# Kernel tuning notes

Measured on AMD Instinct MI355X. Metric: run time of the kernel, lower is better.

The kernel has to match this reference:

```python
import jax, jax.numpy as jnp
import numpy as np

N, D = 8192, 64


def setup_inputs() -> dict:
    key = jax.random.key(0)
    k1, k2, k3 = jax.random.split(key, 3)
    X = jax.random.normal(k1, (N, D), dtype=jnp.float32)
    target = jax.random.normal(k2, (N,), dtype=jnp.float32)
    params = jax.random.uniform(k3, (D,), dtype=jnp.float32)  # positive ARD weights
    return {"X": X, "target": target, "params": params}


def reference(X, target, params):
    # ARD-RBF kernel: k(x, y) = exp(-sum(params * (x - y)^2))
    # = exp(-||xs - ys||^2) with xs = x * sqrt(params)
    Xs = X * jnp.sqrt(params)  # [N, D]
    sq = jnp.sum(Xs * Xs, axis=-1)  # [N]
    d2 = jnp.maximum(sq[:, None] + sq[None, :] - 2.0 * (Xs @ Xs.T), 0.0)  # [N, N]
    K = jnp.exp(-d2)
    # torch version initializes K = eye(N) and never overwrites the diagonal
    n = X.shape[0]
    K = K.at[jnp.arange(n), jnp.arange(n)].set(1.0)
    K_target = jnp.outer(target, target)  # [N, N]
    kta = jnp.sum(K * K_target) / (n * jnp.sqrt(jnp.sum(K * K)))
    return -kta
```

## Files before the change

### kernel.cpp

```cpp
#include <hip/hip_runtime.h>
#include <hip/hip_bf16.h>

#define NROWS 8192
#define DIM 64
#define NT 64
#define NTRI (NT * (NT + 1) / 2)

typedef __attribute__((ext_vector_type(8))) short short8;
typedef __attribute__((ext_vector_type(4))) float f32x4;

static constexpr float LOG2E = 1.4426950408889634f;

#if defined(__has_builtin) && __has_builtin(__builtin_amdgcn_exp2f)
#define EXP2F(x) __builtin_amdgcn_exp2f(x)
#else
#define EXP2F(x) exp2f(x)
#endif

__global__ __launch_bounds__(256) void prep_kernel(const float* __restrict__ X,
                                                   const float* __restrict__ params,
                                                   const float* __restrict__ t,
                                                   float2* __restrict__ Lt,
                                                   short* __restrict__ Xp) {
    int tid  = threadIdx.x;
    int wave = tid >> 6, lane = tid & 63;
    int r8 = lane >> 3, c = lane & 7;
    int row = blockIdx.x * 32 + wave * 8 + r8;

    const float* xr = X + row * DIM + c * 8;
    float4 x0 = *(const float4*)xr;
    float4 x1 = *(const float4*)(xr + 4);
    float4 p0 = *(const float4*)(params + c * 8);
    float4 p1 = *(const float4*)(params + c * 8 + 4);

    float v[8];
    v[0] = x0.x * sqrtf(p0.x); v[1] = x0.y * sqrtf(p0.y);
    v[2] = x0.z * sqrtf(p0.z); v[3] = x0.w * sqrtf(p0.w);
    v[4] = x1.x * sqrtf(p1.x); v[5] = x1.y * sqrtf(p1.y);
    v[6] = x1.z * sqrtf(p1.z); v[7] = x1.w * sqrtf(p1.w);

    short8 h;
    float s = 0.f;
    #pragma unroll
    for (int i = 0; i < 8; ++i) {
        __hip_bfloat16 b = __float2bfloat16(v[i]);
        union { __hip_bfloat16 bb; short ss; } u; u.bb = b;
        h[i] = u.ss;
        float bf = __bfloat162float(b);
        s += bf * bf;
    }
    int panel = row >> 4, pr = row & 15;
    ((short8*)Xp)[panel * 128 + c * 16 + pr] = h;

    #pragma unroll
    for (int m = 1; m < 8; m <<= 1) s += __shfl_xor(s, m, 64);
    if (c == 0) Lt[row] = make_float2(LOG2E * s, t[row]);
}

__global__ __launch_bounds__(256, 4) void kta_main(const short* __restrict__ Xp,
                                                   const float2* __restrict__ Lt,
                                                   float2* __restrict__ partial) {
    int k = blockIdx.x;
    int it = (int)((129.0f - sqrtf(16641.0f - 8.0f * (float)k)) * 0.5f);
    if (it > NT - 1) it = NT - 1;
    while ((it * (129 - it)) / 2 > k) --it;
    while (((it + 1) * (128 - it)) / 2 <= k) ++it;
    int jt = it + (k - (it * (129 - it)) / 2);

    int tid  = threadIdx.x;
    int wave = tid >> 6, lane = tid & 63;
    int quad = lane >> 4, l16 = lane & 15;
    int rbase = it * 128 + (wave >> 1) * 64;
    int cbase = jt * 128 + (wave & 1) * 64;
    int pA0 = rbase >> 4, pB0 = cbase >> 4;

    const short8* Xpv = (const short8*)Xp;

    float negLC[4], tC[4];
    #pragma unroll
    for (int ct = 0; ct < 4; ++ct) {
        float2 lc = Lt[cbase + ct * 16 + l16];
        negLC[ct] = -lc.x;
        tC[ct]    = lc.y;
    }

    f32x4 c[4][4];
    #pragma unroll
    for (int rt = 0; rt < 4; ++rt)
        #pragma unroll
        for (int ct = 0; ct < 4; ++ct)
            c[rt][ct] = (f32x4){0.f, 0.f, 0.f, 0.f};

    #pragma unroll
    for (int kc = 0; kc < 2; ++kc) {
        short8 afr[4], bfr[4];
        #pragma unroll
        for (int rt = 0; rt < 4; ++rt) {
            afr[rt] = Xpv[(pA0 + rt) * 128 + (kc * 4 + quad) * 16 + l16];
            bfr[rt] = Xpv[(pB0 + rt) * 128 + (kc * 4 + quad) * 16 + l16];
        }
        #pragma unroll
        for (int rt = 0; rt < 4; ++rt)
            #pragma unroll
            for (int ct = 0; ct < 4; ++ct)
                c[rt][ct] = __builtin_amdgcn_mfma_f32_16x16x32_bf16(afr[rt], bfr[ct], c[rt][ct], 0, 0, 0);
    }

    float ts1 = 0.f, ts2 = 0.f;
    #pragma unroll
    for (int rt = 0; rt < 4; ++rt) {
        float2 LtR[4];
        #pragma unroll
        for (int r = 0; r < 4; ++r)
            LtR[r] = Lt[rbase + rt * 16 + quad * 4 + r];
        #pragma unroll
        for (int r = 0; r < 4; ++r) {
            float nr = LtR[r].x;
            float s1row = 0.f;
            #pragma unroll
            for (int ct = 0; ct < 4; ++ct) {
                float K = EXP2F(fmaf(c[rt][ct][r], 2.0f * LOG2E, negLC[ct] - nr));
                s1row = fmaf(K, tC[ct], s1row);
                ts2   = fmaf(K, K, ts2);
            }
            ts1 = fmaf(s1row, LtR[r].y, ts1);
        }
    }

    float w = (it == jt) ? 1.0f : 2.0f;
    float s1 = ts1 * w, s2 = ts2 * w;
    #pragma unroll
    for (int m = 32; m > 0; m >>= 1) {
        s1 += __shfl_xor(s1, m, 64);
        s2 += __shfl_xor(s2, m, 64);
    }
    __shared__ float2 red[4];
    if (lane == 0) red[wave] = make_float2(s1, s2);
    __syncthreads();
    if (tid == 0) {
        float2 a = red[0], b = red[1], cc = red[2], d = red[3];
        partial[k] = make_float2(a.x + b.x + cc.x + d.x, a.y + b.y + cc.y + d.y);
    }
}

__global__ __launch_bounds__(256) void finalize_kernel(const float2* __restrict__ partial,
                                                       float* __restrict__ out) {
    float s1 = 0.f, s2 = 0.f;
    for (int i = threadIdx.x; i < NTRI; i += 256) {
        float2 p = partial[i];
        s1 += p.x;
        s2 += p.y;
    }
    #pragma unroll
    for (int m = 32; m > 0; m >>= 1) {
        s1 += __shfl_xor(s1, m, 64);
        s2 += __shfl_xor(s2, m, 64);
    }
    __shared__ float r1[4], r2[4];
    int wave = threadIdx.x >> 6, lane = threadIdx.x & 63;
    if (lane == 0) { r1[wave] = s1; r2[wave] = s2; }
    __syncthreads();
    if (threadIdx.x == 0) {
        float a = r1[0] + r1[1] + r1[2] + r1[3];
        float b = r2[0] + r2[1] + r2[2] + r2[3];
        out[0] = -a / ((float)NROWS * sqrtf(b));
    }
}

extern "C" void kernel_launch(void* const* d_in, const int* in_sizes, int n_in,
                              void* d_out, int out_size, void* d_ws, size_t ws_size,
                              hipStream_t stream) {
    const float* X      = (const float*)d_in[0];
    const float* target = (const float*)d_in[1];
    const float* params = (const float*)d_in[2];
    float* out = (float*)d_out;

    float* ws = (float*)d_ws;
    float2* partial = (float2*)ws;
    float2* Lt = (float2*)(ws + 8192);
    short*  Xp = (short*)(ws + 8192 + 16384);

    prep_kernel<<<NROWS / 32, 256, 0, stream>>>(X, params, target, Lt, Xp);
    kta_main<<<NTRI, 256, 0, stream>>>(Xp, Lt, partial);
    finalize_kernel<<<1, 256, 0, stream>>>(partial, out);
}
```

Measured before the change: 74.89 us.

## Make main kernel persistent with software-prefetched next tile

Replaces the one-block-per-tile launch of 2080 blocks with a persistent grid of 512 blocks that stride over the triangular tile list. Each block prefetches the next tile's A/B fragments and column norms into registers before running the exp epilogue on the current tile, so load latency is hidden behind the epilogue math. Occupancy drops from 4 to 3 blocks per SIMD because the doubled fragment registers add pressure. Tiles are spread unevenly (about 4 per block), and each block now emits a single partial.

```diff
diff --git a/kernel.cpp b/kernel.cpp
--- a/kernel.cpp
+++ b/kernel.cpp
@@ -5,6 +5,7 @@
 #define DIM 64
 #define NT 64
 #define NTRI (NT * (NT + 1) / 2)
+#define GRID 512
 
 typedef __attribute__((ext_vector_type(8))) short short8;
 typedef __attribute__((ext_vector_type(4))) float f32x4;
@@ -57,78 +58,111 @@
     if (c == 0) Lt[row] = make_float2(LOG2E * s, t[row]);
 }
 
-__global__ __launch_bounds__(256, 4) void kta_main(const short* __restrict__ Xp,
+__global__ __launch_bounds__(256, 3) void kta_main(const short* __restrict__ Xp,
                                                    const float2* __restrict__ Lt,
                                                    float2* __restrict__ partial) {
-    int k = blockIdx.x;
-    int it = (int)((129.0f - sqrtf(16641.0f - 8.0f * (float)k)) * 0.5f);
-    if (it > NT - 1) it = NT - 1;
-    while ((it * (129 - it)) / 2 > k) --it;
-    while (((it + 1) * (128 - it)) / 2 <= k) ++it;
-    int jt = it + (k - (it * (129 - it)) / 2);
-
     int tid  = threadIdx.x;
     int wave = tid >> 6, lane = tid & 63;
     int quad = lane >> 4, l16 = lane & 15;
-    int rbase = it * 128 + (wave >> 1) * 64;
-    int cbase = jt * 128 + (wave & 1) * 64;
-    int pA0 = rbase >> 4, pB0 = cbase >> 4;
+    int rsub = (wave >> 1) * 64, csub = (wave & 1) * 64;
 
     const short8* Xpv = (const short8*)Xp;
 
-    float negLC[4], tC[4];
-    #pragma unroll
-    for (int ct = 0; ct < 4; ++ct) {
-        float2 lc = Lt[cbase + ct * 16 + l16];
-        negLC[ct] = -lc.x;
-        tC[ct]    = lc.y;
-    }
-
-    f32x4 c[4][4];
-    #pragma unroll
-    for (int rt = 0; rt < 4; ++rt)
+    auto decode = [](int k, int& it, int& jt) {
+        int i = (int)((129.0f - sqrtf(16641.0f - 8.0f * (float)k)) * 0.5f);
+        if (i > NT - 1) i = NT - 1;
+        while ((i * (129 - i)) / 2 > k) --i;
+        while (((i + 1) * (128 - i)) / 2 <= k) ++i;
+        it = i; jt = i + (k - (i * (129 - i)) / 2);
+    };
+
+    short8 afr[4][2], bfr[4][2];
+    float2 ltc[4];
+    auto load_tile = [&](int rbase, int cbase) {
+        int pA0 = rbase >> 4, pB0 = cbase >> 4;
+        #pragma unroll
+        for (int rt = 0; rt < 4; ++rt) {
+            #pragma unroll
+            for (int kc = 0; kc < 2; ++kc) {
+                afr[rt][kc] = Xpv[(pA0 + rt) * 128 + (kc * 4 + quad) * 16 + l16];
+                bfr[rt][kc] = Xpv[(pB0 + rt) * 128 + (kc * 4 + quad) * 16 + l16];
+            }
+        }
         #pragma unroll
         for (int ct = 0; ct < 4; ++ct)
-            c[rt][ct] = (f32x4){0.f, 0.f, 0.f, 0.f};
-
-    #pragma unroll
-    for (int kc = 0; kc < 2; ++kc) {
-        short8 afr[4], bfr[4];
+            ltc[ct] = Lt[cbase + ct * 16 + l16];
+    };
+
+    float s1 = 0.f, s2 = 0.f;
+    int k = blockIdx.x;
+    int it, jt;
+    decode(k, it, jt);
+    int rbase = it * 128 + rsub, cbase = jt * 128 + csub;
+    float w = (it == jt) ? 1.0f : 2.0f;
+    load_tile(rbase, cbase);
+
+    while (true) {
+        int rb = rbase;
+        float wcur = w;
+
+        f32x4 c[4][4];
+        #pragma unroll
+        for (int rt = 0; rt < 4; ++rt)
+            #pragma unroll
+            for (int ct = 0; ct < 4; ++ct)
+                c[rt][ct] = __builtin_amdgcn_mfma_f32_16x16x32_bf16(
+                    afr[rt][0], bfr[ct][0], (f32x4){0.f, 0.f, 0.f, 0.f}, 0, 0, 0);
+        #pragma unroll
+        for (int rt = 0; rt < 4; ++rt)
+            #pragma unroll
+            for (int ct = 0; ct < 4; ++ct)
+                c[rt][ct] = __builtin_amdgcn_mfma_f32_16x16x32_bf16(
+                    afr[rt][1], bfr[ct][1], c[rt][ct], 0, 0, 0);
+
+        float negLC[4], tC[4];
+        #pragma unroll
+        for (int ct = 0; ct < 4; ++ct) {
+            negLC[ct] = -ltc[ct].x;
+            tC[ct]    = ltc[ct].y;
+        }
+
+        int kn = k + GRID;
+        bool more = (kn < NTRI);
+        if (more) {
+            decode(kn, it, jt);
+            rbase = it * 128 + rsub;
+            cbase = jt * 128 + csub;
+            w = (it == jt) ? 1.0f : 2.0f;
+            load_tile(rbase, cbase);
+        }
+
+        float ts1 = 0.f, ts2 = 0.f;
         #pragma unroll
         for (int rt = 0; rt < 4; ++rt) {
-            afr[rt] = Xpv[(pA0 + rt) * 128 + (kc * 4 + quad) * 16 + l16];
-            bfr[rt] = Xpv[(pB0 + rt) * 128 + (kc * 4 + quad) * 16 + l16];
-        }
-        #pragma unroll
-        for (int rt = 0; rt < 4; ++rt)
-            #pragma unroll
-            for (int ct = 0; ct < 4; ++ct)
-                c[rt][ct] = __builtin_amdgcn_mfma_f32_16x16x32_bf16(afr[rt], bfr[ct], c[rt][ct], 0, 0, 0);
-    }
-
-    float ts1 = 0.f, ts2 = 0.f;
-    #pragma unroll
-    for (int rt = 0; rt < 4; ++rt) {
-        float2 LtR[4];
-        #pragma unroll
-        for (int r = 0; r < 4; ++r)
-            LtR[r] = Lt[rbase + rt * 16 + quad * 4 + r];
-        #pragma unroll
-        for (int r = 0; r < 4; ++r) {
-            float nr = LtR[r].x;
-            float s1row = 0.f;
-            #pragma unroll
-            for (int ct = 0; ct < 4; ++ct) {
-                float K = EXP2F(fmaf(c[rt][ct][r], 2.0f * LOG2E, negLC[ct] - nr));
-                s1row = fmaf(K, tC[ct], s1row);
-                ts2   = fmaf(K, K, ts2);
+            float2 LtR[4];
+            #pragma unroll
+            for (int r = 0; r < 4; ++r)
+                LtR[r] = Lt[rb + rt * 16 + quad * 4 + r];
+            #pragma unroll
+            for (int r = 0; r < 4; ++r) {
+                float nr = LtR[r].x;
+                float s1row = 0.f;
+                #pragma unroll
+                for (int ct = 0; ct < 4; ++ct) {
+                    float K = EXP2F(fmaf(c[rt][ct][r], 2.0f * LOG2E, negLC[ct] - nr));
+                    s1row = fmaf(K, tC[ct], s1row);
+                    ts2   = fmaf(K, K, ts2);
+                }
+                ts1 = fmaf(s1row, LtR[r].y, ts1);
             }
-            ts1 = fmaf(s1row, LtR[r].y, ts1);
-        }
-    }
-
-    float w = (it == jt) ? 1.0f : 2.0f;
-    float s1 = ts1 * w, s2 = ts2 * w;
+        }
+        s1 = fmaf(ts1, wcur, s1);
+        s2 = fmaf(ts2, wcur, s2);
+
+        if (!more) break;
+        k = kn;
+    }
+
     #pragma unroll
     for (int m = 32; m > 0; m >>= 1) {
         s1 += __shfl_xor(s1, m, 64);
@@ -139,14 +173,14 @@
     __syncthreads();
     if (tid == 0) {
         float2 a = red[0], b = red[1], cc = red[2], d = red[3];
-        partial[k] = make_float2(a.x + b.x + cc.x + d.x, a.y + b.y + cc.y + d.y);
+        partial[blockIdx.x] = make_float2(a.x + b.x + cc.x + d.x, a.y + b.y + cc.y + d.y);
     }
 }
 
 __global__ __launch_bounds__(256) void finalize_kernel(const float2* __restrict__ partial,
                                                        float* __restrict__ out) {
     float s1 = 0.f, s2 = 0.f;
-    for (int i = threadIdx.x; i < NTRI; i += 256) {
+    for (int i = threadIdx.x; i < GRID; i += 256) {
         float2 p = partial[i];
         s1 += p.x;
         s2 += p.y;
@@ -181,6 +215,6 @@
     short*  Xp = (short*)(ws + 8192 + 16384);
 
     prep_kernel<<<NROWS / 32, 256, 0, stream>>>(X, params, target, Lt, Xp);
-    kta_main<<<NTRI, 256, 0, stream>>>(Xp, Lt, partial);
+    kta_main<<<GRID, 256, 0, stream>>>(Xp, Lt, partial);
     finalize_kernel<<<1, 256, 0, stream>>>(partial, out);
 }
```

After: 76.55 us. 1.02x slower.
